# Performance work log

Measured on AMD Instinct MI355X. Metric: run time of the kernel, lower is better.

Reference implementation:

```python
import jax, jax.numpy as jnp
import numpy as np

B, T, U, D, V = 8, 256, 64, 640, 1024  # batch, enc frames, target len, per-stream dim, vocab


def setup_inputs() -> dict:
    key = jax.random.key(0)
    k1, k2, k3, k4 = jax.random.split(key, 4)
    return {
        "source_encodings": jax.random.normal(k1, (B, T, D), dtype=jnp.float32),
        "source_lengths": jnp.full((B,), T, dtype=jnp.int32),  # full lengths -> static packed shape
        "target_encodings": jax.random.normal(k2, (B, U, D), dtype=jnp.float32),
        "target_lengths": jnp.full((B,), U, dtype=jnp.int32),
        "W": jax.random.normal(k3, (V, 2 * D), dtype=jnp.float32) / np.sqrt(2 * D).astype(np.float32),
        "b": jax.random.normal(k4, (V,), dtype=jnp.float32) * 0.01,
    }


def reference(source_encodings, source_lengths, target_encodings, target_lengths, W, b):
    # Per-batch broadcast-concat over the (T, U) joint lattice, then flatten rows.
    # With full lengths this equals the torch per-sample loop (same row order).
    enc = jnp.broadcast_to(source_encodings[:, :, None, :], (B, T, U, D))   # [B,T,U,D]
    pred = jnp.broadcast_to(target_encodings[:, None, :, :], (B, T, U, D))  # [B,T,U,D]
    joint_input = jnp.concatenate([enc, pred], axis=-1).reshape(B * T * U, 2 * D)
    # joiner: dropout(p=0 -> identity) -> ReLU -> Linear
    activation_out = jax.nn.relu(joint_input)
    joint_output = activation_out @ W.T + b  # [B*T*U, V]
    return joint_output, source_lengths, target_lengths
```

## Files before the change

### kernel.cpp

```cpp
#include <hip/hip_runtime.h>


typedef float floatx4 __attribute__((ext_vector_type(4)));

#define PBM 64
#define PBN 64
#define PBK 16
#define PPAD 4

__global__ __launch_bounds__(256) void p_gemm_kernel(
    const float* __restrict__ pred,
    const float* __restrict__ W,
    float* __restrict__ P)
{
    __shared__ float As[PBK][PBM + PPAD];
    __shared__ float Bs[PBK][PBN + PPAD];

    const int tid  = threadIdx.x;
    const int row0 = blockIdx.y * PBM;
    const int col0 = blockIdx.x * PBN;

    const int lm = tid >> 2;
    const int lk = (tid & 3) * 4;
    const int tx = tid & 15;
    const int ty = tid >> 4;

    float acc[4][4];
    #pragma unroll
    for (int i = 0; i < 4; ++i)
        #pragma unroll
        for (int j = 0; j < 4; ++j) acc[i][j] = 0.f;

    for (int k0 = 0; k0 < 640; k0 += PBK) {
        float4 a4 = *(const float4*)(pred + (size_t)(row0 + lm) * 640 + k0 + lk);
        float4 b4 = *(const float4*)(W + (size_t)(col0 + lm) * 1280 + 640 + k0 + lk);
        As[lk + 0][lm] = fmaxf(a4.x, 0.f);
        As[lk + 1][lm] = fmaxf(a4.y, 0.f);
        As[lk + 2][lm] = fmaxf(a4.z, 0.f);
        As[lk + 3][lm] = fmaxf(a4.w, 0.f);
        Bs[lk + 0][lm] = b4.x;
        Bs[lk + 1][lm] = b4.y;
        Bs[lk + 2][lm] = b4.z;
        Bs[lk + 3][lm] = b4.w;
        __syncthreads();

        #pragma unroll
        for (int k = 0; k < PBK; ++k) {
            float4 av = *(const float4*)&As[k][ty * 4];
            float4 bv = *(const float4*)&Bs[k][tx * 4];
            float ar[4] = {av.x, av.y, av.z, av.w};
            float br[4] = {bv.x, bv.y, bv.z, bv.w};
            #pragma unroll
            for (int i = 0; i < 4; ++i)
                #pragma unroll
                for (int j = 0; j < 4; ++j)
                    acc[i][j] = fmaf(ar[i], br[j], acc[i][j]);
        }
        __syncthreads();
    }

    #pragma unroll
    for (int i = 0; i < 4; ++i) {
        float4 o;
        o.x = acc[i][0]; o.y = acc[i][1]; o.z = acc[i][2]; o.w = acc[i][3];
        *(float4*)(P + (size_t)(row0 + ty * 4 + i) * 1024 + col0 + tx * 4) = o;
    }
}


#define TT 16
#define VT 256
#define KB 16

__global__ __launch_bounds__(128) void e_fused_kernel(
    const float* __restrict__ enc,
    const float* __restrict__ W,
    const float* __restrict__ bias,
    const float* __restrict__ P,
    float* __restrict__ out)
{
    __shared__ float As[KB][TT];
    __shared__ float Ws[KB][VT];

    const int t   = threadIdx.x;
    const int vt  = blockIdx.x;
    const int tt  = blockIdx.y;
    const int bt0 = tt * TT;
    const int v0  = vt * VT;
    const int b   = bt0 >> 8;

    const int w  = t >> 6;
    const int l  = t & 63;
    const int w8 = w * 8;
    const int l4 = l * 4;

    float acc[8][4];
    #pragma unroll
    for (int i = 0; i < 8; ++i)
        #pragma unroll
        for (int j = 0; j < 4; ++j) acc[i][j] = 0.f;

    for (int k0 = 0; k0 < 640; k0 += KB) {
        if (t < 64) {
            const int row = t & 15;
            const int kq  = t >> 4;
            float4 a4 = *(const float4*)(enc + (size_t)(bt0 + row) * 640 + k0 + kq * 4);
            As[kq * 4 + 0][row] = fmaxf(a4.x, 0.f);
            As[kq * 4 + 1][row] = fmaxf(a4.y, 0.f);
            As[kq * 4 + 2][row] = fmaxf(a4.z, 0.f);
            As[kq * 4 + 3][row] = fmaxf(a4.w, 0.f);
        }
        #pragma unroll
        for (int p = 0; p < 2; ++p) {
            const int vv = t * 2 + p;
            const float* wp = W + (size_t)(v0 + vv) * 1280 + k0;
            float4 q0 = ((const float4*)wp)[0];
            float4 q1 = ((const float4*)wp)[1];
            float4 q2 = ((const float4*)wp)[2];
            float4 q3 = ((const float4*)wp)[3];
            Ws[ 0][vv] = q0.x; Ws[ 1][vv] = q0.y; Ws[ 2][vv] = q0.z; Ws[ 3][vv] = q0.w;
            Ws[ 4][vv] = q1.x; Ws[ 5][vv] = q1.y; Ws[ 6][vv] = q1.z; Ws[ 7][vv] = q1.w;
            Ws[ 8][vv] = q2.x; Ws[ 9][vv] = q2.y; Ws[10][vv] = q2.z; Ws[11][vv] = q2.w;
            Ws[12][vv] = q3.x; Ws[13][vv] = q3.y; Ws[14][vv] = q3.z; Ws[15][vv] = q3.w;
        }
        __syncthreads();

        #pragma unroll
        for (int k = 0; k < KB; ++k) {
            float4 a0 = *(const float4*)&As[k][w8];
            float4 a1 = *(const float4*)&As[k][w8 + 4];
            float4 bv = *(const float4*)&Ws[k][l4];
            float ar[8] = {a0.x, a0.y, a0.z, a0.w, a1.x, a1.y, a1.z, a1.w};
            float br[4] = {bv.x, bv.y, bv.z, bv.w};
            #pragma unroll
            for (int i = 0; i < 8; ++i)
                #pragma unroll
                for (int j = 0; j < 4; ++j)
                    acc[i][j] = fmaf(ar[i], br[j], acc[i][j]);
        }
        __syncthreads();
    }

    {
        float4 bb = *(const float4*)(bias + v0 + l4);
        #pragma unroll
        for (int i = 0; i < 8; ++i) {
            acc[i][0] += bb.x; acc[i][1] += bb.y; acc[i][2] += bb.z; acc[i][3] += bb.w;
        }
    }

    const float* Pb = P + (size_t)b * 65536 + v0 + l4;
    float* ob = out + (size_t)(bt0 + w8) * 65536 + v0 + l4;

    #pragma unroll 4
    for (int u = 0; u < 64; ++u) {
        float4 p4 = *(const float4*)(Pb + (size_t)u * 1024);
        #pragma unroll
        for (int i = 0; i < 8; ++i) {
            floatx4 o;
            o.x = acc[i][0] + p4.x;
            o.y = acc[i][1] + p4.y;
            o.z = acc[i][2] + p4.z;
            o.w = acc[i][3] + p4.w;
            __builtin_nontemporal_store(o, (floatx4*)(ob + (size_t)i * 65536 + (size_t)u * 1024));
        }
    }
}

__global__ void lengths_kernel(const int* __restrict__ sl,
                               const int* __restrict__ tl,
                               float* __restrict__ out_tail)
{
    const int i = threadIdx.x;
    if (i < 8) {
        out_tail[i]     = (float)sl[i];
        out_tail[8 + i] = (float)tl[i];
    }
}

extern "C" void kernel_launch(void* const* d_in, const int* in_sizes, int n_in,
                              void* d_out, int out_size, void* d_ws, size_t ws_size,
                              hipStream_t stream) {
    const float* enc  = (const float*)d_in[0];
    const int*   sl   = (const int*)d_in[1];
    const float* pred = (const float*)d_in[2];
    const int*   tl   = (const int*)d_in[3];
    const float* W    = (const float*)d_in[4];
    const float* bias = (const float*)d_in[5];

    float* out = (float*)d_out;
    float* P   = (float*)d_ws;

    p_gemm_kernel<<<dim3(16, 8), 256, 0, stream>>>(pred, W, P);

    e_fused_kernel<<<dim3(4, 128), 128, 0, stream>>>(enc, W, bias, P, out);

    lengths_kernel<<<1, 64, 0, stream>>>(sl, tl, out + (size_t)131072 * 1024);
}
```

Baseline: 668.1 us.

## Enlarge encoder GEMM tile, prefetch next k-slice into registers, use plain stores

The encoder-side fused kernel moves to 256-thread blocks covering 32 frames by 256 vocab columns, halving the grid. The next K-slice of W and enc is loaded into registers while the current slice is computed, and the W shared tile is padded to cut bank conflicts on the transposed writes. The output epilogue now uses ordinary float4 stores instead of nontemporal stores. The kernel is dominated by writing the 512 MB output, so the GEMM changes may matter little, and dropping nontemporal stores could add cache pollution.

```diff
diff --git a/kernel.cpp b/kernel.cpp
--- a/kernel.cpp
+++ b/kernel.cpp
@@ -1,7 +1,5 @@
 #include <hip/hip_runtime.h>
 
-
-typedef float floatx4 __attribute__((ext_vector_type(4)));
 
 #define PBM 64
 #define PBN 64
@@ -68,31 +66,45 @@
 }
 
 
-#define TT 16
-#define VT 256
-#define KB 16
-
-__global__ __launch_bounds__(128) void e_fused_kernel(
+#define EBM 32
+#define EBN 256
+#define EBK 16
+#define WSS 260
+
+__global__ __launch_bounds__(256) void e_fused_kernel(
     const float* __restrict__ enc,
     const float* __restrict__ W,
     const float* __restrict__ bias,
     const float* __restrict__ P,
     float* __restrict__ out)
 {
-    __shared__ float As[KB][TT];
-    __shared__ float Ws[KB][VT];
+    __shared__ float Ws[EBK * WSS];
+    __shared__ float As[EBK * EBM];
 
     const int t   = threadIdx.x;
     const int vt  = blockIdx.x;
     const int tt  = blockIdx.y;
-    const int bt0 = tt * TT;
-    const int v0  = vt * VT;
+    const int bt0 = tt * EBM;
+    const int v0  = vt * EBN;
     const int b   = bt0 >> 8;
 
-    const int w  = t >> 6;
-    const int l  = t & 63;
-    const int w8 = w * 8;
-    const int l4 = l * 4;
+    const int tx = t & 63;
+    const int ty = t >> 6;
+    const int l4 = tx * 4;
+
+    const int svv = t >> 2;
+    const int skc = (t & 3) * 4;
+    const int arow = t & 31;
+    const int akq  = (t >> 5) & 3;
+
+    float4 wq[4];
+    float4 aq = make_float4(0.f, 0.f, 0.f, 0.f);
+
+    #pragma unroll
+    for (int rep = 0; rep < 4; ++rep)
+        wq[rep] = *(const float4*)(W + (size_t)(v0 + rep * 64 + svv) * 1280 + skc);
+    if (t < 128)
+        aq = *(const float4*)(enc + (size_t)(bt0 + arow) * 640 + akq * 4);
 
     float acc[8][4];
     #pragma unroll
@@ -100,49 +112,50 @@
         #pragma unroll
         for (int j = 0; j < 4; ++j) acc[i][j] = 0.f;
 
-    for (int k0 = 0; k0 < 640; k0 += KB) {
-        if (t < 64) {
-            const int row = t & 15;
-            const int kq  = t >> 4;
-            float4 a4 = *(const float4*)(enc + (size_t)(bt0 + row) * 640 + k0 + kq * 4);
-            As[kq * 4 + 0][row] = fmaxf(a4.x, 0.f);
-            As[kq * 4 + 1][row] = fmaxf(a4.y, 0.f);
-            As[kq * 4 + 2][row] = fmaxf(a4.z, 0.f);
-            As[kq * 4 + 3][row] = fmaxf(a4.w, 0.f);
-        }
-        #pragma unroll
-        for (int p = 0; p < 2; ++p) {
-            const int vv = t * 2 + p;
-            const float* wp = W + (size_t)(v0 + vv) * 1280 + k0;
-            float4 q0 = ((const float4*)wp)[0];
-            float4 q1 = ((const float4*)wp)[1];
-            float4 q2 = ((const float4*)wp)[2];
-            float4 q3 = ((const float4*)wp)[3];
-            Ws[ 0][vv] = q0.x; Ws[ 1][vv] = q0.y; Ws[ 2][vv] = q0.z; Ws[ 3][vv] = q0.w;
-            Ws[ 4][vv] = q1.x; Ws[ 5][vv] = q1.y; Ws[ 6][vv] = q1.z; Ws[ 7][vv] = q1.w;
-            Ws[ 8][vv] = q2.x; Ws[ 9][vv] = q2.y; Ws[10][vv] = q2.z; Ws[11][vv] = q2.w;
-            Ws[12][vv] = q3.x; Ws[13][vv] = q3.y; Ws[14][vv] = q3.z; Ws[15][vv] = q3.w;
-        }
-        __syncthreads();
-
-        #pragma unroll
-        for (int k = 0; k < KB; ++k) {
-            float4 a0 = *(const float4*)&As[k][w8];
-            float4 a1 = *(const float4*)&As[k][w8 + 4];
-            float4 bv = *(const float4*)&Ws[k][l4];
-            float ar[8] = {a0.x, a0.y, a0.z, a0.w, a1.x, a1.y, a1.z, a1.w};
-            float br[4] = {bv.x, bv.y, bv.z, bv.w};
+    for (int kt = 0; kt < 40; ++kt) {
+        __syncthreads();
+        #pragma unroll
+        for (int rep = 0; rep < 4; ++rep) {
+            const int vv = rep * 64 + svv;
+            Ws[(skc + 0) * WSS + vv] = wq[rep].x;
+            Ws[(skc + 1) * WSS + vv] = wq[rep].y;
+            Ws[(skc + 2) * WSS + vv] = wq[rep].z;
+            Ws[(skc + 3) * WSS + vv] = wq[rep].w;
+        }
+        if (t < 128) {
+            As[(akq * 4 + 0) * EBM + arow] = fmaxf(aq.x, 0.f);
+            As[(akq * 4 + 1) * EBM + arow] = fmaxf(aq.y, 0.f);
+            As[(akq * 4 + 2) * EBM + arow] = fmaxf(aq.z, 0.f);
+            As[(akq * 4 + 3) * EBM + arow] = fmaxf(aq.w, 0.f);
+        }
+        __syncthreads();
+
+        if (kt + 1 < 40) {
+            const int k0 = (kt + 1) * EBK;
+            #pragma unroll
+            for (int rep = 0; rep < 4; ++rep)
+                wq[rep] = *(const float4*)(W + (size_t)(v0 + rep * 64 + svv) * 1280 + k0 + skc);
+            if (t < 128)
+                aq = *(const float4*)(enc + (size_t)(bt0 + arow) * 640 + k0 + akq * 4);
+        }
+
+        #pragma unroll
+        for (int k = 0; k < EBK; ++k) {
+            const float4 a0 = *(const float4*)&As[k * EBM + ty * 8];
+            const float4 a1 = *(const float4*)&As[k * EBM + ty * 8 + 4];
+            const float4 bv = *(const float4*)&Ws[k * WSS + l4];
+            const float ar[8] = {a0.x, a0.y, a0.z, a0.w, a1.x, a1.y, a1.z, a1.w};
+            const float br[4] = {bv.x, bv.y, bv.z, bv.w};
             #pragma unroll
             for (int i = 0; i < 8; ++i)
                 #pragma unroll
                 for (int j = 0; j < 4; ++j)
                     acc[i][j] = fmaf(ar[i], br[j], acc[i][j]);
         }
-        __syncthreads();
     }
 
     {
-        float4 bb = *(const float4*)(bias + v0 + l4);
+        const float4 bb = *(const float4*)(bias + v0 + l4);
         #pragma unroll
         for (int i = 0; i < 8; ++i) {
             acc[i][0] += bb.x; acc[i][1] += bb.y; acc[i][2] += bb.z; acc[i][3] += bb.w;
@@ -150,19 +163,19 @@
     }
 
     const float* Pb = P + (size_t)b * 65536 + v0 + l4;
-    float* ob = out + (size_t)(bt0 + w8) * 65536 + v0 + l4;
+    float* ob = out + (size_t)(bt0 + ty * 8) * 65536 + v0 + l4;
 
     #pragma unroll 4
     for (int u = 0; u < 64; ++u) {
-        float4 p4 = *(const float4*)(Pb + (size_t)u * 1024);
+        const float4 p4 = *(const float4*)(Pb + (size_t)u * 1024);
         #pragma unroll
         for (int i = 0; i < 8; ++i) {
-            floatx4 o;
+            float4 o;
             o.x = acc[i][0] + p4.x;
             o.y = acc[i][1] + p4.y;
             o.z = acc[i][2] + p4.z;
             o.w = acc[i][3] + p4.w;
-            __builtin_nontemporal_store(o, (floatx4*)(ob + (size_t)i * 65536 + (size_t)u * 1024));
+            *(float4*)(ob + (size_t)i * 65536 + (size_t)u * 1024) = o;
         }
     }
 }
@@ -193,7 +206,7 @@
 
     p_gemm_kernel<<<dim3(16, 8), 256, 0, stream>>>(pred, W, P);
 
-    e_fused_kernel<<<dim3(4, 128), 128, 0, stream>>>(enc, W, bias, P, out);
+    e_fused_kernel<<<dim3(4, 64), 256, 0, stream>>>(enc, W, bias, P, out);
 
     lengths_kernel<<<1, 64, 0, stream>>>(sl, tl, out + (size_t)131072 * 1024);
 }
```

Result: slower. 689.2 us (+3.2%).
